# Kernel tuning notes

Measured on AMD Instinct MI355X. Metric: run time of the kernel, lower is better.

## Reference

```python
import jax, jax.numpy as jnp
import numpy as np

MARGIN = 0.3

def setup_inputs() -> dict:
    key = jax.random.key(0)
    k1, k2 = jax.random.split(key)
    z1 = jax.random.normal(k1, (8192, 128), dtype=jnp.float32)
    z2 = jax.random.normal(k2, (8192, 128), dtype=jnp.float32)
    return {"z1": z1, "z2": z2}

def _cdist(z1, z2):
    # Euclidean pairwise distances via the GEMM identity, avoiding the
    # [N, N, d] broadcasted intermediate. Clamp for numerical safety.
    sq1 = jnp.sum(z1 * z1, axis=1, keepdims=True)        # [N, 1]
    sq2 = jnp.sum(z2 * z2, axis=1, keepdims=True).T      # [1, N]
    d2 = sq1 + sq2 - 2.0 * (z1 @ z2.T)                   # [N, N]
    return jnp.sqrt(jnp.maximum(d2, 0.0))

def reference(z1, z2) -> jnp.ndarray:
    n = z1.shape[0]
    dist = _cdist(z1, z2)                                # [N, N]
    pos_dist = jnp.diagonal(dist)                        # [N]
    # hard negative mining: mask diagonal with +inf, take row-min
    eye = jnp.eye(n, dtype=bool)
    neg_dist = jnp.where(eye, jnp.inf, dist)
    hard_neg = jnp.min(neg_dist, axis=1)                 # [N]
    loss = jax.nn.relu(pos_dist - hard_neg + MARGIN)
    return jnp.mean(loss)
```

## Files before the change

kernel.cpp:

```cpp
#include <hip/hip_runtime.h>

#define MARGIN 0.3f

typedef __attribute__((ext_vector_type(8))) short short8;
typedef __attribute__((ext_vector_type(4))) float floatx4;


__device__ __forceinline__ unsigned enc_f32(float f) {
    unsigned u = __float_as_uint(f);
    return (u & 0x80000000u) ? ~u : (u | 0x80000000u);
}
__device__ __forceinline__ float dec_f32(unsigned u) {
    return (u & 0x80000000u) ? __uint_as_float(u & 0x7fffffffu)
                             : __uint_as_float(~u);
}
__device__ __forceinline__ short f2bf(float f) {
    unsigned u = __float_as_uint(f);
    u = u + 0x7fffu + ((u >> 16) & 1u);
    return (short)(u >> 16);
}


__global__ void prep_kernel(const float* __restrict__ z1, const float* __restrict__ z2,
                            short* __restrict__ z1b, short* __restrict__ z2b,
                            float* __restrict__ sq1, float* __restrict__ sq2,
                            float* __restrict__ posd, unsigned* __restrict__ rowmin,
                            unsigned* __restrict__ cnt, float* __restrict__ out) {
    int h = blockIdx.x * 256 + threadIdx.x;
    int row = h >> 4, p = h & 15;
    int kk = p >> 2, q = p & 3;
    int f0 = row * 32 + kk * 8 + q * 2;
    float4 fa0 = ((const float4*)z1)[f0], fa1 = ((const float4*)z1)[f0 + 1];
    float4 fb0 = ((const float4*)z2)[f0], fb1 = ((const float4*)z2)[f0 + 1];
    short8 sa = { f2bf(fa0.x), f2bf(fa0.y), f2bf(fa0.z), f2bf(fa0.w),
                  f2bf(fa1.x), f2bf(fa1.y), f2bf(fa1.z), f2bf(fa1.w) };
    short8 sb = { f2bf(fb0.x), f2bf(fb0.y), f2bf(fb0.z), f2bf(fb0.w),
                  f2bf(fb1.x), f2bf(fb1.y), f2bf(fb1.z), f2bf(fb1.w) };
    size_t off = (size_t)(row >> 4) * 2048 + kk * 512 + q * 128 + (row & 15) * 8;
    *(short8*)&z1b[off] = sa;
    *(short8*)&z2b[off] = sb;

    float s1 = fa0.x*fa0.x + fa0.y*fa0.y + fa0.z*fa0.z + fa0.w*fa0.w
             + fa1.x*fa1.x + fa1.y*fa1.y + fa1.z*fa1.z + fa1.w*fa1.w;
    float s2 = fb0.x*fb0.x + fb0.y*fb0.y + fb0.z*fb0.z + fb0.w*fb0.w
             + fb1.x*fb1.x + fb1.y*fb1.y + fb1.z*fb1.z + fb1.w*fb1.w;
    float dx0 = fa0.x-fb0.x, dy0 = fa0.y-fb0.y, dz0 = fa0.z-fb0.z, dw0 = fa0.w-fb0.w;
    float dx1 = fa1.x-fb1.x, dy1 = fa1.y-fb1.y, dz1 = fa1.z-fb1.z, dw1 = fa1.w-fb1.w;
    float p2 = dx0*dx0 + dy0*dy0 + dz0*dz0 + dw0*dw0
             + dx1*dx1 + dy1*dy1 + dz1*dz1 + dw1*dw1;
    #pragma unroll
    for (int m = 8; m >= 1; m >>= 1) {
        s1 += __shfl_xor(s1, m);
        s2 += __shfl_xor(s2, m);
        p2 += __shfl_xor(p2, m);
    }
    if (p == 0) { sq1[row] = s1; sq2[row] = s2; posd[row] = sqrtf(p2); }

    if (threadIdx.x < 16) rowmin[blockIdx.x * 16 + threadIdx.x] = 0xFFFFFFFFu;
    if (blockIdx.x == 0) {
        if (threadIdx.x < 32) cnt[threadIdx.x] = 0u;
        if (threadIdx.x == 0) out[0] = 0.0f;
    }
}

__global__ __launch_bounds__(256, 2)
void gemm_min_kernel(const short* __restrict__ z1b, const short* __restrict__ z2b,
                     const float* __restrict__ sq1, const float* __restrict__ sq2,
                     const float* __restrict__ posd,
                     unsigned* __restrict__ rowmin, unsigned* __restrict__ cnt,
                     float* __restrict__ out, int n)
{
    __shared__ float lsum[4];
    __shared__ int   fin_s;

    const int rg = blockIdx.y, cgi = blockIdx.x;
    const int tid = threadIdx.x, w = tid >> 6, lane = tid & 63;
    const int quad = lane >> 4, l15 = lane & 15;
    const int rowbase = rg * 256 + w * 64;
    const int colorig = cgi * 512;

    short8 af[4][4];
    #pragma unroll
    for (int sm = 0; sm < 4; ++sm) {
        const short* pa = z1b + (size_t)(rg * 16 + w * 4 + sm) * 2048 + lane * 8;
        #pragma unroll
        for (int kk = 0; kk < 4; ++kk)
            af[sm][kk] = *(const short8*)(pa + kk * 512);
    }

    float vmin[4][4];
    #pragma unroll
    for (int sm = 0; sm < 4; ++sm)
        #pragma unroll
        for (int reg = 0; reg < 4; ++reg)
            vmin[sm][reg] = 3.0e38f;

    short8 bb[2][2][4];
    #pragma unroll
    for (int sn = 0; sn < 2; ++sn) {
        const short* pb = z2b + (size_t)(cgi * 32 + sn) * 2048 + lane * 8;
        #pragma unroll
        for (int kk = 0; kk < 4; ++kk)
            bb[0][sn][kk] = *(const short8*)(pb + kk * 512);
    }

    #pragma unroll
    for (int t = 0; t < 16; ++t) {
        if (t < 15) {
            #pragma unroll
            for (int sn = 0; sn < 2; ++sn) {
                const short* pb = z2b + (size_t)(cgi * 32 + (t + 1) * 2 + sn) * 2048 + lane * 8;
                #pragma unroll
                for (int kk = 0; kk < 4; ++kk)
                    bb[(t + 1) & 1][sn][kk] = *(const short8*)(pb + kk * 512);
            }
        }
        const int colbase = colorig + t * 32;
        float s2v0 = sq2[colbase + l15];
        float s2v1 = sq2[colbase + 16 + l15];

        floatx4 acc[4][2];
        #pragma unroll
        for (int sm = 0; sm < 4; ++sm)
            #pragma unroll
            for (int sn = 0; sn < 2; ++sn)
                acc[sm][sn] = (floatx4)0.0f;

        #pragma unroll
        for (int kk = 0; kk < 4; ++kk)
            #pragma unroll
            for (int sm = 0; sm < 4; ++sm)
                #pragma unroll
                for (int sn = 0; sn < 2; ++sn)
                    acc[sm][sn] = __builtin_amdgcn_mfma_f32_16x16x32_bf16(
                        af[sm][kk], bb[t & 1][sn][kk], acc[sm][sn], 0, 0, 0);

        if (colbase < rowbase + 64 && rowbase < colbase + 32) {
            #pragma unroll
            for (int sm = 0; sm < 4; ++sm)
                #pragma unroll
                for (int reg = 0; reg < 4; ++reg) {
                    int gi = rowbase + sm * 16 + quad * 4 + reg;
                    float v0 = fmaf(-2.0f, acc[sm][0][reg], s2v0);
                    float v1 = fmaf(-2.0f, acc[sm][1][reg], s2v1);
                    v0 = (gi == colbase + l15)      ? 3.0e38f : v0;
                    v1 = (gi == colbase + 16 + l15) ? 3.0e38f : v1;
                    vmin[sm][reg] = fminf(vmin[sm][reg], fminf(v0, v1));
                }
        } else {
            #pragma unroll
            for (int sm = 0; sm < 4; ++sm)
                #pragma unroll
                for (int reg = 0; reg < 4; ++reg) {
                    float v0 = fmaf(-2.0f, acc[sm][0][reg], s2v0);
                    float v1 = fmaf(-2.0f, acc[sm][1][reg], s2v1);
                    vmin[sm][reg] = fminf(vmin[sm][reg], fminf(v0, v1));
                }
        }
    }

    #pragma unroll
    for (int sm = 0; sm < 4; ++sm)
        #pragma unroll
        for (int reg = 0; reg < 4; ++reg) {
            float vm = vmin[sm][reg];
            #pragma unroll
            for (int m = 8; m >= 1; m >>= 1)
                vm = fminf(vm, __shfl_xor(vm, m));
            if (l15 == 0)
                atomicMin(&rowmin[rowbase + sm * 16 + quad * 4 + reg], enc_f32(vm));
        }

    __syncthreads();
    if (tid == 0) {
        __threadfence();
        fin_s = (atomicAdd(&cnt[rg], 1u) == 15u);
    }
    __syncthreads();
    if (!fin_s) return;
    __threadfence();

    {
        int i = rg * 256 + tid;
        unsigned rm = atomicMin(&rowmin[i], 0xFFFFFFFFu);
        float hard = sqrtf(fmaxf(sq1[i] + dec_f32(rm), 0.0f));
        float l = fmaxf(posd[i] - hard + MARGIN, 0.0f);
        #pragma unroll
        for (int m = 32; m >= 1; m >>= 1) l += __shfl_xor(l, m);
        if (lane == 0) lsum[w] = l;
    }
    __syncthreads();
    if (tid == 0)
        atomicAdd(out, (lsum[0] + lsum[1] + lsum[2] + lsum[3]) / (float)n);
}

extern "C" void kernel_launch(void* const* d_in, const int* in_sizes, int n_in,
                              void* d_out, int out_size, void* d_ws, size_t ws_size,
                              hipStream_t stream) {
    const float* z1 = (const float*)d_in[0];
    const float* z2 = (const float*)d_in[1];
    const int n = in_sizes[0] / 128;

    char* ws = (char*)d_ws;
    short*    z1b    = (short*)ws;
    short*    z2b    = (short*)(ws + (size_t)n * 128 * 2);
    float*    sq1    = (float*)(ws + (size_t)n * 128 * 4);
    float*    sq2    = (float*)(ws + (size_t)n * 128 * 4 + n * 4);
    float*    posd   = (float*)(ws + (size_t)n * 128 * 4 + n * 8);
    unsigned* rowmin = (unsigned*)(ws + (size_t)n * 128 * 4 + n * 12);
    unsigned* cnt    = (unsigned*)(ws + (size_t)n * 128 * 4 + n * 16);
    float*    out    = (float*)d_out;

    prep_kernel<<<n / 16, 256, 0, stream>>>(z1, z2, z1b, z2b, sq1, sq2, posd,
                                            rowmin, cnt, out);
    dim3 grid(16, n / 256);
    gemm_min_kernel<<<grid, 256, 0, stream>>>(z1b, z2b, sq1, sq2, posd,
                                              rowmin, cnt, out, n);
}
```

Before: 103.9 us.

## Stage B tiles and column norms in LDS via async global-to-LDS loads

Each wave used to load its own copy of the z2 bf16 tiles straight from global memory into registers. Now the block cooperatively streams 64-column B chunks into double-buffered shared memory with global_load_lds, and every wave reads them from LDS, so the four waves share each global load. The sq2 column norms are also staged once into LDS. This adds about 33KB of LDS per block and a barrier per chunk, which may limit occupancy or stall the waves on synchronisation.

```diff
diff --git a/kernel.cpp b/kernel.cpp
--- a/kernel.cpp
+++ b/kernel.cpp
@@ -18,6 +18,12 @@
     unsigned u = __float_as_uint(f);
     u = u + 0x7fffu + ((u >> 16) & 1u);
     return (short)(u >> 16);
+}
+
+__device__ __forceinline__ void gload_lds16(const void* g, void* l) {
+    __builtin_amdgcn_global_load_lds(
+        (const __attribute__((address_space(1))) void*)g,
+        (__attribute__((address_space(3))) void*)l, 16, 0, 0);
 }
 
 
@@ -70,6 +76,8 @@
                      unsigned* __restrict__ rowmin, unsigned* __restrict__ cnt,
                      float* __restrict__ out, int n)
 {
+    __shared__ __align__(16) short sb[2][8192];
+    __shared__ __align__(16) float s2l[512];
     __shared__ float lsum[4];
     __shared__ int   fin_s;
 
@@ -79,6 +87,13 @@
     const int rowbase = rg * 256 + w * 64;
     const int colorig = cgi * 512;
 
+    if (tid < 128)
+        gload_lds16(sq2 + colorig + tid * 4, s2l + tid * 4);
+    const short* gb = z2b + (size_t)(cgi * 32) * 2048;
+    #pragma unroll
+    for (int o = 0; o < 4; ++o)
+        gload_lds16(gb + (tid + o * 256) * 8, &sb[0][(tid + o * 256) * 8]);
+
     short8 af[4][4];
     #pragma unroll
     for (int sm = 0; sm < 4; ++sm) {
@@ -95,67 +110,75 @@
         for (int reg = 0; reg < 4; ++reg)
             vmin[sm][reg] = 3.0e38f;
 
-    short8 bb[2][2][4];
-    #pragma unroll
-    for (int sn = 0; sn < 2; ++sn) {
-        const short* pb = z2b + (size_t)(cgi * 32 + sn) * 2048 + lane * 8;
-        #pragma unroll
-        for (int kk = 0; kk < 4; ++kk)
-            bb[0][sn][kk] = *(const short8*)(pb + kk * 512);
-    }
-
-    #pragma unroll
-    for (int t = 0; t < 16; ++t) {
-        if (t < 15) {
-            #pragma unroll
-            for (int sn = 0; sn < 2; ++sn) {
-                const short* pb = z2b + (size_t)(cgi * 32 + (t + 1) * 2 + sn) * 2048 + lane * 8;
+    #pragma unroll 1
+    for (int s = 0; s < 8; ++s) {
+        asm volatile("s_waitcnt vmcnt(0)" ::: "memory");
+        __builtin_amdgcn_s_barrier();
+        __builtin_amdgcn_sched_barrier(0);
+        asm volatile("" ::: "memory");
+
+        if (s < 7) {
+            const short* src = gb + (size_t)(s + 1) * 8192;
+            short* dst = &sb[(s + 1) & 1][0];
+            #pragma unroll
+            for (int o = 0; o < 4; ++o)
+                gload_lds16(src + (tid + o * 256) * 8, dst + (tid + o * 256) * 8);
+        }
+
+        const short* bs = &sb[s & 1][0];
+        #pragma unroll
+        for (int hf = 0; hf < 2; ++hf) {
+            const int tcol = s * 64 + hf * 32;
+            const int colbase = colorig + tcol;
+            const float s2v0 = s2l[tcol + l15];
+            const float s2v1 = s2l[tcol + 16 + l15];
+
+            short8 bq[2][4];
+            #pragma unroll
+            for (int sn = 0; sn < 2; ++sn)
                 #pragma unroll
                 for (int kk = 0; kk < 4; ++kk)
-                    bb[(t + 1) & 1][sn][kk] = *(const short8*)(pb + kk * 512);
+                    bq[sn][kk] = *(const short8*)(bs + hf * 4096 + sn * 2048
+                                                  + kk * 512 + lane * 8);
+
+            floatx4 acc[4][2];
+            #pragma unroll
+            for (int sm = 0; sm < 4; ++sm)
+                #pragma unroll
+                for (int sn = 0; sn < 2; ++sn)
+                    acc[sm][sn] = (floatx4)0.0f;
+
+            #pragma unroll
+            for (int kk = 0; kk < 4; ++kk)
+                #pragma unroll
+                for (int sm = 0; sm < 4; ++sm)
+                    #pragma unroll
+                    for (int sn = 0; sn < 2; ++sn)
+                        acc[sm][sn] = __builtin_amdgcn_mfma_f32_16x16x32_bf16(
+                            af[sm][kk], bq[sn][kk], acc[sm][sn], 0, 0, 0);
+
+            if (colbase < rowbase + 64 && rowbase < colbase + 32) {
+                #pragma unroll
+                for (int sm = 0; sm < 4; ++sm)
+                    #pragma unroll
+                    for (int reg = 0; reg < 4; ++reg) {
+                        int gi = rowbase + sm * 16 + quad * 4 + reg;
+                        float v0 = fmaf(-2.0f, acc[sm][0][reg], s2v0);
+                        float v1 = fmaf(-2.0f, acc[sm][1][reg], s2v1);
+                        v0 = (gi == colbase + l15)      ? 3.0e38f : v0;
+                        v1 = (gi == colbase + 16 + l15) ? 3.0e38f : v1;
+                        vmin[sm][reg] = fminf(vmin[sm][reg], fminf(v0, v1));
+                    }
+            } else {
+                #pragma unroll
+                for (int sm = 0; sm < 4; ++sm)
+                    #pragma unroll
+                    for (int reg = 0; reg < 4; ++reg) {
+                        float v0 = fmaf(-2.0f, acc[sm][0][reg], s2v0);
+                        float v1 = fmaf(-2.0f, acc[sm][1][reg], s2v1);
+                        vmin[sm][reg] = fminf(vmin[sm][reg], fminf(v0, v1));
+                    }
             }
-        }
-        const int colbase = colorig + t * 32;
-        float s2v0 = sq2[colbase + l15];
-        float s2v1 = sq2[colbase + 16 + l15];
-
-        floatx4 acc[4][2];
-        #pragma unroll
-        for (int sm = 0; sm < 4; ++sm)
-            #pragma unroll
-            for (int sn = 0; sn < 2; ++sn)
-                acc[sm][sn] = (floatx4)0.0f;
-
-        #pragma unroll
-        for (int kk = 0; kk < 4; ++kk)
-            #pragma unroll
-            for (int sm = 0; sm < 4; ++sm)
-                #pragma unroll
-                for (int sn = 0; sn < 2; ++sn)
-                    acc[sm][sn] = __builtin_amdgcn_mfma_f32_16x16x32_bf16(
-                        af[sm][kk], bb[t & 1][sn][kk], acc[sm][sn], 0, 0, 0);
-
-        if (colbase < rowbase + 64 && rowbase < colbase + 32) {
-            #pragma unroll
-            for (int sm = 0; sm < 4; ++sm)
-                #pragma unroll
-                for (int reg = 0; reg < 4; ++reg) {
-                    int gi = rowbase + sm * 16 + quad * 4 + reg;
-                    float v0 = fmaf(-2.0f, acc[sm][0][reg], s2v0);
-                    float v1 = fmaf(-2.0f, acc[sm][1][reg], s2v1);
-                    v0 = (gi == colbase + l15)      ? 3.0e38f : v0;
-                    v1 = (gi == colbase + 16 + l15) ? 3.0e38f : v1;
-                    vmin[sm][reg] = fminf(vmin[sm][reg], fminf(v0, v1));
-                }
-        } else {
-            #pragma unroll
-            for (int sm = 0; sm < 4; ++sm)
-                #pragma unroll
-                for (int reg = 0; reg < 4; ++reg) {
-                    float v0 = fmaf(-2.0f, acc[sm][0][reg], s2v0);
-                    float v1 = fmaf(-2.0f, acc[sm][1][reg], s2v1);
-                    vmin[sm][reg] = fminf(vmin[sm][reg], fminf(v0, v1));
-                }
         }
     }
 
```

Result: faster. 91.08 us (-12.3%).

## Stage shared B tiles in LDS via direct global-to-LDS loads and double the grid

Applied to the files above, without the earlier changes.

Each block now stages its 256-column slice of bf16 z2 and the matching squared norms into LDS with asynchronous global_load_lds. The loads are split into four stages, each gated by a vmcnt wait and a barrier, so all four waves read B from LDS instead of each fetching it from global memory. The column tile per block is halved and the grid becomes 32x32 blocks, which raises parallelism and changes the last-block counter threshold from 15 to 31. In exchange it uses about 65 KB of LDS per block, which may limit how many blocks fit per CU. It also relies on hand-counted vmcnt values that must match the exact issue order of the loads.

```diff
diff --git a/kernel.cpp b/kernel.cpp
--- a/kernel.cpp
+++ b/kernel.cpp
@@ -18,6 +18,17 @@
     unsigned u = __float_as_uint(f);
     u = u + 0x7fffu + ((u >> 16) & 1u);
     return (short)(u >> 16);
+}
+
+__device__ __forceinline__ void gload_lds16(const void* g, void* l) {
+    __builtin_amdgcn_global_load_lds(
+        (const __attribute__((address_space(1))) void*)g,
+        (__attribute__((address_space(3))) void*)l, 16, 0, 0);
+}
+__device__ __forceinline__ void gload_lds4(const void* g, void* l) {
+    __builtin_amdgcn_global_load_lds(
+        (const __attribute__((address_space(1))) void*)g,
+        (__attribute__((address_space(3))) void*)l, 4, 0, 0);
 }
 
 
@@ -70,6 +81,8 @@
                      unsigned* __restrict__ rowmin, unsigned* __restrict__ cnt,
                      float* __restrict__ out, int n)
 {
+    __shared__ __align__(16) short sb[4][8192];
+    __shared__ __align__(16) float s2l[256];
     __shared__ float lsum[4];
     __shared__ int   fin_s;
 
@@ -77,7 +90,16 @@
     const int tid = threadIdx.x, w = tid >> 6, lane = tid & 63;
     const int quad = lane >> 4, l15 = lane & 15;
     const int rowbase = rg * 256 + w * 64;
-    const int colorig = cgi * 512;
+    const int colorig = cgi * 256;
+
+    const short* gb = z2b + (size_t)(cgi * 16) * 2048;
+
+    #pragma unroll
+    for (int o = 0; o < 4; ++o)
+        gload_lds16(gb + (tid + o * 256) * 8, &sb[0][(tid + o * 256) * 8]);
+    __builtin_amdgcn_sched_barrier(0);
+    gload_lds4(sq2 + colorig + tid, &s2l[tid]);
+    __builtin_amdgcn_sched_barrier(0);
 
     short8 af[4][4];
     #pragma unroll
@@ -87,6 +109,15 @@
         for (int kk = 0; kk < 4; ++kk)
             af[sm][kk] = *(const short8*)(pa + kk * 512);
     }
+    __builtin_amdgcn_sched_barrier(0);
+    #pragma unroll
+    for (int s = 1; s < 4; ++s) {
+        #pragma unroll
+        for (int o = 0; o < 4; ++o)
+            gload_lds16(gb + (size_t)s * 8192 + (tid + o * 256) * 8,
+                        &sb[s][(tid + o * 256) * 8]);
+        __builtin_amdgcn_sched_barrier(0);
+    }
 
     float vmin[4][4];
     #pragma unroll
@@ -95,69 +126,70 @@
         for (int reg = 0; reg < 4; ++reg)
             vmin[sm][reg] = 3.0e38f;
 
-    short8 bb[2][2][4];
-    #pragma unroll
-    for (int sn = 0; sn < 2; ++sn) {
-        const short* pb = z2b + (size_t)(cgi * 32 + sn) * 2048 + lane * 8;
-        #pragma unroll
-        for (int kk = 0; kk < 4; ++kk)
-            bb[0][sn][kk] = *(const short8*)(pb + kk * 512);
-    }
-
-    #pragma unroll
-    for (int t = 0; t < 16; ++t) {
-        if (t < 15) {
-            #pragma unroll
-            for (int sn = 0; sn < 2; ++sn) {
-                const short* pb = z2b + (size_t)(cgi * 32 + (t + 1) * 2 + sn) * 2048 + lane * 8;
-                #pragma unroll
-                for (int kk = 0; kk < 4; ++kk)
-                    bb[(t + 1) & 1][sn][kk] = *(const short8*)(pb + kk * 512);
-            }
-        }
-        const int colbase = colorig + t * 32;
-        float s2v0 = sq2[colbase + l15];
-        float s2v1 = sq2[colbase + 16 + l15];
-
-        floatx4 acc[4][2];
-        #pragma unroll
-        for (int sm = 0; sm < 4; ++sm)
-            #pragma unroll
-            for (int sn = 0; sn < 2; ++sn)
-                acc[sm][sn] = (floatx4)0.0f;
-
-        #pragma unroll
-        for (int kk = 0; kk < 4; ++kk)
-            #pragma unroll
-            for (int sm = 0; sm < 4; ++sm)
-                #pragma unroll
-                for (int sn = 0; sn < 2; ++sn)
-                    acc[sm][sn] = __builtin_amdgcn_mfma_f32_16x16x32_bf16(
-                        af[sm][kk], bb[t & 1][sn][kk], acc[sm][sn], 0, 0, 0);
-
-        if (colbase < rowbase + 64 && rowbase < colbase + 32) {
-            #pragma unroll
-            for (int sm = 0; sm < 4; ++sm)
-                #pragma unroll
-                for (int reg = 0; reg < 4; ++reg) {
-                    int gi = rowbase + sm * 16 + quad * 4 + reg;
-                    float v0 = fmaf(-2.0f, acc[sm][0][reg], s2v0);
-                    float v1 = fmaf(-2.0f, acc[sm][1][reg], s2v1);
-                    v0 = (gi == colbase + l15)      ? 3.0e38f : v0;
-                    v1 = (gi == colbase + 16 + l15) ? 3.0e38f : v1;
-                    vmin[sm][reg] = fminf(vmin[sm][reg], fminf(v0, v1));
-                }
-        } else {
-            #pragma unroll
-            for (int sm = 0; sm < 4; ++sm)
-                #pragma unroll
-                for (int reg = 0; reg < 4; ++reg) {
-                    float v0 = fmaf(-2.0f, acc[sm][0][reg], s2v0);
-                    float v1 = fmaf(-2.0f, acc[sm][1][reg], s2v1);
-                    vmin[sm][reg] = fminf(vmin[sm][reg], fminf(v0, v1));
-                }
-        }
-    }
+#define SUPERPHASE(S, VMTXT)                                                   \
+    do {                                                                       \
+        asm volatile("s_waitcnt vmcnt(" VMTXT ")" ::: "memory");               \
+        __builtin_amdgcn_sched_barrier(0);                                     \
+        __builtin_amdgcn_s_barrier();                                          \
+        __builtin_amdgcn_sched_barrier(0);                                     \
+        const short* bs_ = &sb[S][0];                                          \
+        _Pragma("unroll")                                                      \
+        for (int hf = 0; hf < 2; ++hf) {                                       \
+            const int tcol = (S) * 64 + hf * 32;                               \
+            const int colbase = colorig + tcol;                                \
+            const float s2v0 = s2l[tcol + l15];                                \
+            const float s2v1 = s2l[tcol + 16 + l15];                           \
+            short8 bq[2][4];                                                   \
+            _Pragma("unroll")                                                  \
+            for (int sn = 0; sn < 2; ++sn)                                     \
+                _Pragma("unroll")                                              \
+                for (int kk = 0; kk < 4; ++kk)                                 \
+                    bq[sn][kk] = *(const short8*)(bs_ + hf * 4096 + sn * 2048  \
+                                                  + kk * 512 + lane * 8);      \
+            floatx4 acc[4][2];                                                 \
+            _Pragma("unroll")                                                  \
+            for (int sm = 0; sm < 4; ++sm)                                     \
+                _Pragma("unroll")                                              \
+                for (int sn = 0; sn < 2; ++sn)                                 \
+                    acc[sm][sn] = (floatx4)0.0f;                               \
+            _Pragma("unroll")                                                  \
+            for (int kk = 0; kk < 4; ++kk)                                     \
+                _Pragma("unroll")                                              \
+                for (int sm = 0; sm < 4; ++sm)                                 \
+                    _Pragma("unroll")                                          \
+                    for (int sn = 0; sn < 2; ++sn)                             \
+                        acc[sm][sn] = __builtin_amdgcn_mfma_f32_16x16x32_bf16( \
+                            af[sm][kk], bq[sn][kk], acc[sm][sn], 0, 0, 0);     \
+            if (colbase < rowbase + 64 && rowbase < colbase + 32) {            \
+                _Pragma("unroll")                                              \
+                for (int sm = 0; sm < 4; ++sm)                                 \
+                    _Pragma("unroll")                                          \
+                    for (int reg = 0; reg < 4; ++reg) {                        \
+                        int gi = rowbase + sm * 16 + quad * 4 + reg;           \
+                        float v0 = fmaf(-2.0f, acc[sm][0][reg], s2v0);         \
+                        float v1 = fmaf(-2.0f, acc[sm][1][reg], s2v1);         \
+                        v0 = (gi == colbase + l15)      ? 3.0e38f : v0;        \
+                        v1 = (gi == colbase + 16 + l15) ? 3.0e38f : v1;        \
+                        vmin[sm][reg] = fminf(vmin[sm][reg], fminf(v0, v1));   \
+                    }                                                          \
+            } else {                                                           \
+                _Pragma("unroll")                                              \
+                for (int sm = 0; sm < 4; ++sm)                                 \
+                    _Pragma("unroll")                                          \
+                    for (int reg = 0; reg < 4; ++reg) {                        \
+                        float v0 = fmaf(-2.0f, acc[sm][0][reg], s2v0);         \
+                        float v1 = fmaf(-2.0f, acc[sm][1][reg], s2v1);         \
+                        vmin[sm][reg] = fminf(vmin[sm][reg], fminf(v0, v1));   \
+                    }                                                          \
+            }                                                                  \
+        }                                                                      \
+    } while (0)
+
+    SUPERPHASE(0, "12");
+    SUPERPHASE(1, "8");
+    SUPERPHASE(2, "4");
+    SUPERPHASE(3, "0");
+#undef SUPERPHASE
 
     #pragma unroll
     for (int sm = 0; sm < 4; ++sm)
@@ -174,7 +206,7 @@
     __syncthreads();
     if (tid == 0) {
         __threadfence();
-        fin_s = (atomicAdd(&cnt[rg], 1u) == 15u);
+        fin_s = (atomicAdd(&cnt[rg], 1u) == 31u);
     }
     __syncthreads();
     if (!fin_s) return;
@@ -213,7 +245,7 @@
 
     prep_kernel<<<n / 16, 256, 0, stream>>>(z1, z2, z1b, z2b, sq1, sq2, posd,
                                             rowmin, cnt, out);
-    dim3 grid(16, n / 256);
+    dim3 grid(n / 256, n / 256);
     gemm_min_kernel<<<grid, 256, 0, stream>>>(z1b, z2b, sq1, sq2, posd,
                                               rowmin, cnt, out, n);
 }
```

Result: slower. 109.9 us (+5.8%).

## Fuse bf16 conversion and norms into GEMM-min kernel with LDS-staged B tiles

Applied to the files above, without the earlier changes.

Removes the separate prep kernel and computes the bf16 conversion, squared norms and positive distances inside the main kernel. The z2 column tile is staged in LDS already scaled by -2, and sq2 is preloaded into the accumulators to save epilogue FMAs. Blocks grow to 512 threads over 512x512 tiles with an XCD-aware block index remap, and MFMA priority is raised. The cost is redundant fp32 reads of z1 per column block, 128KB of LDS per block limiting occupancy, and a fixed 256-block grid.

```diff
diff --git a/kernel.cpp b/kernel.cpp
--- a/kernel.cpp
+++ b/kernel.cpp
@@ -20,73 +20,101 @@
     return (short)(u >> 16);
 }
 
-
-__global__ void prep_kernel(const float* __restrict__ z1, const float* __restrict__ z2,
-                            short* __restrict__ z1b, short* __restrict__ z2b,
-                            float* __restrict__ sq1, float* __restrict__ sq2,
-                            float* __restrict__ posd, unsigned* __restrict__ rowmin,
-                            unsigned* __restrict__ cnt, float* __restrict__ out) {
-    int h = blockIdx.x * 256 + threadIdx.x;
-    int row = h >> 4, p = h & 15;
-    int kk = p >> 2, q = p & 3;
-    int f0 = row * 32 + kk * 8 + q * 2;
-    float4 fa0 = ((const float4*)z1)[f0], fa1 = ((const float4*)z1)[f0 + 1];
-    float4 fb0 = ((const float4*)z2)[f0], fb1 = ((const float4*)z2)[f0 + 1];
-    short8 sa = { f2bf(fa0.x), f2bf(fa0.y), f2bf(fa0.z), f2bf(fa0.w),
-                  f2bf(fa1.x), f2bf(fa1.y), f2bf(fa1.z), f2bf(fa1.w) };
-    short8 sb = { f2bf(fb0.x), f2bf(fb0.y), f2bf(fb0.z), f2bf(fb0.w),
-                  f2bf(fb1.x), f2bf(fb1.y), f2bf(fb1.z), f2bf(fb1.w) };
-    size_t off = (size_t)(row >> 4) * 2048 + kk * 512 + q * 128 + (row & 15) * 8;
-    *(short8*)&z1b[off] = sa;
-    *(short8*)&z2b[off] = sb;
-
-    float s1 = fa0.x*fa0.x + fa0.y*fa0.y + fa0.z*fa0.z + fa0.w*fa0.w
-             + fa1.x*fa1.x + fa1.y*fa1.y + fa1.z*fa1.z + fa1.w*fa1.w;
-    float s2 = fb0.x*fb0.x + fb0.y*fb0.y + fb0.z*fb0.z + fb0.w*fb0.w
-             + fb1.x*fb1.x + fb1.y*fb1.y + fb1.z*fb1.z + fb1.w*fb1.w;
-    float dx0 = fa0.x-fb0.x, dy0 = fa0.y-fb0.y, dz0 = fa0.z-fb0.z, dw0 = fa0.w-fb0.w;
-    float dx1 = fa1.x-fb1.x, dy1 = fa1.y-fb1.y, dz1 = fa1.z-fb1.z, dw1 = fa1.w-fb1.w;
-    float p2 = dx0*dx0 + dy0*dy0 + dz0*dz0 + dw0*dw0
-             + dx1*dx1 + dy1*dy1 + dz1*dz1 + dw1*dw1;
-    #pragma unroll
-    for (int m = 8; m >= 1; m >>= 1) {
-        s1 += __shfl_xor(s1, m);
-        s2 += __shfl_xor(s2, m);
-        p2 += __shfl_xor(p2, m);
-    }
-    if (p == 0) { sq1[row] = s1; sq2[row] = s2; posd[row] = sqrtf(p2); }
-
-    if (threadIdx.x < 16) rowmin[blockIdx.x * 16 + threadIdx.x] = 0xFFFFFFFFu;
+__global__ void init_kernel(unsigned* __restrict__ rowmin, unsigned* __restrict__ cnt,
+                            float* __restrict__ out) {
+    int i = blockIdx.x * 512 + threadIdx.x;
+    rowmin[i] = 0xFFFFFFFFu;
     if (blockIdx.x == 0) {
         if (threadIdx.x < 32) cnt[threadIdx.x] = 0u;
         if (threadIdx.x == 0) out[0] = 0.0f;
     }
 }
 
-__global__ __launch_bounds__(256, 2)
-void gemm_min_kernel(const short* __restrict__ z1b, const short* __restrict__ z2b,
-                     const float* __restrict__ sq1, const float* __restrict__ sq2,
-                     const float* __restrict__ posd,
-                     unsigned* __restrict__ rowmin, unsigned* __restrict__ cnt,
-                     float* __restrict__ out, int n)
+__global__ __launch_bounds__(512, 2)
+void fused_kernel(const float* __restrict__ z1, const float* __restrict__ z2,
+                  float* __restrict__ posd,
+                  unsigned* __restrict__ rowmin, unsigned* __restrict__ cnt,
+                  float* __restrict__ out, int n)
 {
-    __shared__ float lsum[4];
+    __shared__ __align__(16) short bt[65536];
+    __shared__ __align__(16) float s2l[512];
+    __shared__ __align__(16) float sq1l[512];
+    __shared__ float lsum[8];
     __shared__ int   fin_s;
 
-    const int rg = blockIdx.y, cgi = blockIdx.x;
+    const int bid = blockIdx.x;
+    const int xcd = bid & 7, idx = bid >> 3;
+    const int rg  = (xcd << 1) | (idx >> 4);
+    const int cgi = idx & 15;
+
     const int tid = threadIdx.x, w = tid >> 6, lane = tid & 63;
     const int quad = lane >> 4, l15 = lane & 15;
-    const int rowbase = rg * 256 + w * 64;
+    const int rowbase = rg * 512 + w * 64;
     const int colorig = cgi * 512;
 
+    {
+        const float4* zb = (const float4*)(z2 + (size_t)(colorig + tid) * 128);
+        float s2 = 0.f;
+        #pragma unroll
+        for (int kk = 0; kk < 4; ++kk) {
+            float4 f[8];
+            #pragma unroll
+            for (int j = 0; j < 8; ++j) f[j] = zb[kk * 8 + j];
+            #pragma unroll
+            for (int j = 0; j < 8; ++j)
+                s2 += f[j].x*f[j].x + f[j].y*f[j].y + f[j].z*f[j].z + f[j].w*f[j].w;
+            #pragma unroll
+            for (int q = 0; q < 4; ++q) {
+                float4 a = f[q * 2], b = f[q * 2 + 1];
+                short8 sc = { f2bf(-2.f*a.x), f2bf(-2.f*a.y), f2bf(-2.f*a.z), f2bf(-2.f*a.w),
+                              f2bf(-2.f*b.x), f2bf(-2.f*b.y), f2bf(-2.f*b.z), f2bf(-2.f*b.w) };
+                *(short8*)&bt[(tid >> 4) * 2048 + kk * 512 + q * 128 + (tid & 15) * 8] = sc;
+            }
+        }
+        s2l[tid] = s2;
+    }
+
     short8 af[4][4];
-    #pragma unroll
-    for (int sm = 0; sm < 4; ++sm) {
-        const short* pa = z1b + (size_t)(rg * 16 + w * 4 + sm) * 2048 + lane * 8;
-        #pragma unroll
-        for (int kk = 0; kk < 4; ++kk)
-            af[sm][kk] = *(const short8*)(pa + kk * 512);
-    }
+    {
+        float s1p[4] = {0.f, 0.f, 0.f, 0.f};
+        #pragma unroll
+        for (int sm = 0; sm < 4; ++sm) {
+            const float4* zr = (const float4*)(z1 + (size_t)(rowbase + sm * 16 + l15) * 128);
+            #pragma unroll
+            for (int kk = 0; kk < 4; ++kk) {
+                float4 u0 = zr[kk * 8 + quad * 2];
+                float4 u1 = zr[kk * 8 + quad * 2 + 1];
+                s1p[sm] += u0.x*u0.x + u0.y*u0.y + u0.z*u0.z + u0.w*u0.w
+                         + u1.x*u1.x + u1.y*u1.y + u1.z*u1.z + u1.w*u1.w;
+                af[sm][kk] = { f2bf(u0.x), f2bf(u0.y), f2bf(u0.z), f2bf(u0.w),
+                               f2bf(u1.x), f2bf(u1.y), f2bf(u1.z), f2bf(u1.w) };
+            }
+        }
+        #pragma unroll
+        for (int sm = 0; sm < 4; ++sm) {
+            float s1 = s1p[sm];
+            s1 += __shfl_xor(s1, 16);
+            s1 += __shfl_xor(s1, 32);
+            if (quad == 0) sq1l[w * 64 + sm * 16 + l15] = s1;
+        }
+    }
+
+    {
+        int ri = rg * 512 + cgi * 32 + (tid >> 4);
+        int e  = (tid & 15) * 8;
+        const float4* p1 = (const float4*)(z1 + (size_t)ri * 128 + e);
+        const float4* p2 = (const float4*)(z2 + (size_t)ri * 128 + e);
+        float4 a0 = p1[0], a1 = p1[1], b0 = p2[0], b1 = p2[1];
+        float dx0 = a0.x-b0.x, dy0 = a0.y-b0.y, dz0 = a0.z-b0.z, dw0 = a0.w-b0.w;
+        float dx1 = a1.x-b1.x, dy1 = a1.y-b1.y, dz1 = a1.z-b1.z, dw1 = a1.w-b1.w;
+        float p2a = dx0*dx0 + dy0*dy0 + dz0*dz0 + dw0*dw0
+                  + dx1*dx1 + dy1*dy1 + dz1*dz1 + dw1*dw1;
+        #pragma unroll
+        for (int m = 8; m >= 1; m >>= 1) p2a += __shfl_xor(p2a, m);
+        if ((tid & 15) == 0) posd[ri] = sqrtf(p2a);
+    }
+
+    __syncthreads();
 
     float vmin[4][4];
     #pragma unroll
@@ -95,67 +123,64 @@
         for (int reg = 0; reg < 4; ++reg)
             vmin[sm][reg] = 3.0e38f;
 
-    short8 bb[2][2][4];
     #pragma unroll
-    for (int sn = 0; sn < 2; ++sn) {
-        const short* pb = z2b + (size_t)(cgi * 32 + sn) * 2048 + lane * 8;
-        #pragma unroll
-        for (int kk = 0; kk < 4; ++kk)
-            bb[0][sn][kk] = *(const short8*)(pb + kk * 512);
-    }
-
-    #pragma unroll
-    for (int t = 0; t < 16; ++t) {
-        if (t < 15) {
-            #pragma unroll
-            for (int sn = 0; sn < 2; ++sn) {
-                const short* pb = z2b + (size_t)(cgi * 32 + (t + 1) * 2 + sn) * 2048 + lane * 8;
+    for (int S = 0; S < 8; ++S) {
+        const short* bs_ = &bt[S * 8192];
+        #pragma unroll
+        for (int hf = 0; hf < 2; ++hf) {
+            const int tcol = S * 64 + hf * 32;
+            const int colbase = colorig + tcol;
+            const float s2v0 = s2l[tcol + l15];
+            const float s2v1 = s2l[tcol + 16 + l15];
+
+            short8 bq[2][4];
+            #pragma unroll
+            for (int sn = 0; sn < 2; ++sn)
                 #pragma unroll
                 for (int kk = 0; kk < 4; ++kk)
-                    bb[(t + 1) & 1][sn][kk] = *(const short8*)(pb + kk * 512);
+                    bq[sn][kk] = *(const short8*)(bs_ + hf * 4096 + sn * 2048
+                                                  + kk * 512 + lane * 8);
+
+            floatx4 acc[4][2];
+            #pragma unroll
+            for (int sm = 0; sm < 4; ++sm)
+                #pragma unroll
+                for (int reg = 0; reg < 4; ++reg) {
+                    acc[sm][0][reg] = s2v0;
+                    acc[sm][1][reg] = s2v1;
+                }
+
+            __builtin_amdgcn_s_setprio(1);
+            #pragma unroll
+            for (int kk = 0; kk < 4; ++kk)
+                #pragma unroll
+                for (int sm = 0; sm < 4; ++sm)
+                    #pragma unroll
+                    for (int sn = 0; sn < 2; ++sn)
+                        acc[sm][sn] = __builtin_amdgcn_mfma_f32_16x16x32_bf16(
+                            af[sm][kk], bq[sn][kk], acc[sm][sn], 0, 0, 0);
+            __builtin_amdgcn_s_setprio(0);
+
+            if (colbase < rowbase + 64 && rowbase < colbase + 32) {
+                #pragma unroll
+                for (int sm = 0; sm < 4; ++sm)
+                    #pragma unroll
+                    for (int reg = 0; reg < 4; ++reg) {
+                        int gi = rowbase + sm * 16 + quad * 4 + reg;
+                        float v0 = acc[sm][0][reg];
+                        float v1 = acc[sm][1][reg];
+                        v0 = (gi == colbase + l15)      ? 3.0e38f : v0;
+                        v1 = (gi == colbase + 16 + l15) ? 3.0e38f : v1;
+                        vmin[sm][reg] = fminf(vmin[sm][reg], fminf(v0, v1));
+                    }
+            } else {
+                #pragma unroll
+                for (int sm = 0; sm < 4; ++sm)
+                    #pragma unroll
+                    for (int reg = 0; reg < 4; ++reg)
+                        vmin[sm][reg] = fminf(vmin[sm][reg],
+                            fminf(acc[sm][0][reg], acc[sm][1][reg]));
             }
-        }
-        const int colbase = colorig + t * 32;
-        float s2v0 = sq2[colbase + l15];
-        float s2v1 = sq2[colbase + 16 + l15];
-
-        floatx4 acc[4][2];
-        #pragma unroll
-        for (int sm = 0; sm < 4; ++sm)
-            #pragma unroll
-            for (int sn = 0; sn < 2; ++sn)
-                acc[sm][sn] = (floatx4)0.0f;
-
-        #pragma unroll
-        for (int kk = 0; kk < 4; ++kk)
-            #pragma unroll
-            for (int sm = 0; sm < 4; ++sm)
-                #pragma unroll
-                for (int sn = 0; sn < 2; ++sn)
-                    acc[sm][sn] = __builtin_amdgcn_mfma_f32_16x16x32_bf16(
-                        af[sm][kk], bb[t & 1][sn][kk], acc[sm][sn], 0, 0, 0);
-
-        if (colbase < rowbase + 64 && rowbase < colbase + 32) {
-            #pragma unroll
-            for (int sm = 0; sm < 4; ++sm)
-                #pragma unroll
-                for (int reg = 0; reg < 4; ++reg) {
-                    int gi = rowbase + sm * 16 + quad * 4 + reg;
-                    float v0 = fmaf(-2.0f, acc[sm][0][reg], s2v0);
-                    float v1 = fmaf(-2.0f, acc[sm][1][reg], s2v1);
-                    v0 = (gi == colbase + l15)      ? 3.0e38f : v0;
-                    v1 = (gi == colbase + 16 + l15) ? 3.0e38f : v1;
-                    vmin[sm][reg] = fminf(vmin[sm][reg], fminf(v0, v1));
-                }
-        } else {
-            #pragma unroll
-            for (int sm = 0; sm < 4; ++sm)
-                #pragma unroll
-                for (int reg = 0; reg < 4; ++reg) {
-                    float v0 = fmaf(-2.0f, acc[sm][0][reg], s2v0);
-                    float v1 = fmaf(-2.0f, acc[sm][1][reg], s2v1);
-                    vmin[sm][reg] = fminf(vmin[sm][reg], fminf(v0, v1));
-                }
         }
     }
 
@@ -181,17 +206,21 @@
     __threadfence();
 
     {
-        int i = rg * 256 + tid;
+        int i = rg * 512 + tid;
         unsigned rm = atomicMin(&rowmin[i], 0xFFFFFFFFu);
-        float hard = sqrtf(fmaxf(sq1[i] + dec_f32(rm), 0.0f));
+        float hard = sqrtf(fmaxf(sq1l[tid] + dec_f32(rm), 0.0f));
         float l = fmaxf(posd[i] - hard + MARGIN, 0.0f);
         #pragma unroll
         for (int m = 32; m >= 1; m >>= 1) l += __shfl_xor(l, m);
         if (lane == 0) lsum[w] = l;
     }
     __syncthreads();
-    if (tid == 0)
-        atomicAdd(out, (lsum[0] + lsum[1] + lsum[2] + lsum[3]) / (float)n);
+    if (tid == 0) {
+        float t = 0.f;
+        #pragma unroll
+        for (int i = 0; i < 8; ++i) t += lsum[i];
+        atomicAdd(out, t / (float)n);
+    }
 }
 
 extern "C" void kernel_launch(void* const* d_in, const int* in_sizes, int n_in,
@@ -202,18 +231,12 @@
     const int n = in_sizes[0] / 128;
 
     char* ws = (char*)d_ws;
-    short*    z1b    = (short*)ws;
-    short*    z2b    = (short*)(ws + (size_t)n * 128 * 2);
-    float*    sq1    = (float*)(ws + (size_t)n * 128 * 4);
-    float*    sq2    = (float*)(ws + (size_t)n * 128 * 4 + n * 4);
-    float*    posd   = (float*)(ws + (size_t)n * 128 * 4 + n * 8);
-    unsigned* rowmin = (unsigned*)(ws + (size_t)n * 128 * 4 + n * 12);
-    unsigned* cnt    = (unsigned*)(ws + (size_t)n * 128 * 4 + n * 16);
+    float*    posd   = (float*)ws;
+    unsigned* rowmin = (unsigned*)(ws + (size_t)n * 4);
+    unsigned* cnt    = (unsigned*)(ws + (size_t)n * 8);
     float*    out    = (float*)d_out;
 
-    prep_kernel<<<n / 16, 256, 0, stream>>>(z1, z2, z1b, z2b, sq1, sq2, posd,
-                                            rowmin, cnt, out);
-    dim3 grid(16, n / 256);
-    gemm_min_kernel<<<grid, 256, 0, stream>>>(z1b, z2b, sq1, sq2, posd,
-                                              rowmin, cnt, out, n);
-}
+    init_kernel<<<n / 512, 512, 0, stream>>>(rowmin, cnt, out);
+    fused_kernel<<<(n / 512) * (n / 512), 512, 0, stream>>>(
+        z1, z2, posd, rowmin, cnt, out, n);
+}
```

Result: faster. 96.30 us (-7.3%).
